# Kernel optimization log

Hardware: AMD Instinct MI355X
Metric: run time of the kernel (lower is better)

Reference implementation:

```python
import jax, jax.numpy as jnp
import numpy as np

B, T, C, H = 64, 512, 384, 64

def setup_inputs() -> dict:
    key = jax.random.key(0)
    ks = jax.random.split(key, 7)
    s = 0.02
    return {
        "x": jax.random.normal(ks[0], (B, T, C), dtype=jnp.float32),
        "Wq": jax.random.normal(ks[1], (C, H), dtype=jnp.float32) * s,
        "bq": jax.random.normal(ks[2], (H,), dtype=jnp.float32) * s,
        "Wk": jax.random.normal(ks[3], (C, H), dtype=jnp.float32) * s,
        "bk": jax.random.normal(ks[4], (H,), dtype=jnp.float32) * s,
        "Wv": jax.random.normal(ks[5], (C, H), dtype=jnp.float32) * s,
        "bv": jax.random.normal(ks[6], (H,), dtype=jnp.float32) * s,
    }

def reference(x, Wq, bq, Wk, bk, Wv, bv):
    # single-head causal self-attention (dropout in eval mode -> identity)
    q = x @ Wq + bq                      # [B,T,H]
    k = x @ Wk + bk                      # [B,T,H]
    v = x @ Wv + bv                      # [B,T,H]
    scale = jnp.asarray(k.shape[-1], x.dtype) ** -0.5
    scores = jnp.einsum('bth,bsh->bts', q, k) * scale   # [B,T,T]
    t = scores.shape[-1]
    causal = jnp.tril(jnp.ones((t, t), dtype=bool))
    scores = jnp.where(causal, scores, jnp.asarray(-jnp.inf, scores.dtype))
    attn = jax.nn.softmax(scores, axis=-1)               # [B,T,T]
    out = jnp.einsum('bts,bsh->bth', attn, v)            # [B,T,H]
    return out
```

## Files before the change

### kernel.cpp

```cpp
#include <hip/hip_runtime.h>
#include <math.h>

#define BB 64
#define TT 512
#define CC 384
#define HH 64
#define MM (BB*TT)

#define QSCALE 0.18033688011112042f

typedef __attribute__((ext_vector_type(8))) short short8;
typedef __attribute__((ext_vector_type(4))) float f32x4;

__device__ __forceinline__ unsigned short f2bf(float f) {
    union { float f; unsigned int u; } x; x.f = f;
    unsigned int r = x.u + 0x7fff + ((x.u >> 16) & 1);
    return (unsigned short)(r >> 16);
}

__global__ __launch_bounds__(256) void prep_w(
    const float* __restrict__ Wq, const float* __restrict__ Wk,
    const float* __restrict__ Wv, unsigned short* __restrict__ Wt)
{
    __shared__ float t[64][65];
    const int which = blockIdx.x / 6;
    const int kt    = blockIdx.x % 6;
    const float* W = (which == 0) ? Wq : (which == 1) ? Wk : Wv;
    const float sc = (which == 0) ? QSCALE : 1.f;
    const int tid = threadIdx.x;
    #pragma unroll
    for (int i = 0; i < 16; i++) {
        int idx = tid + i * 256;
        int kl = idx >> 6, n = idx & 63;
        t[kl][n] = W[(size_t)(kt * 64 + kl) * HH + n];
    }
    __syncthreads();
    #pragma unroll
    for (int i = 0; i < 16; i++) {
        int idx = tid + i * 256;
        int nl = idx >> 6, kl = idx & 63;
        Wt[(size_t)(which * 64 + nl) * CC + kt * 64 + kl] = f2bf(t[kl][nl] * sc);
    }
}

__global__ __launch_bounds__(256) void qkv_proj_mfma(
    const float* __restrict__ x, const unsigned short* __restrict__ Wt,
    const float* __restrict__ bq, const float* __restrict__ bk,
    const float* __restrict__ bv,
    unsigned short* __restrict__ qb, unsigned short* __restrict__ kb,
    unsigned short* __restrict__ vt)
{
    __shared__ unsigned short xs[64][CC + 8];
    const int tid  = threadIdx.x;
    const int w    = tid >> 6;
    const int lane = tid & 63;
    const int l15  = lane & 15;
    const int lg   = lane >> 4;
    const int rows0 = blockIdx.x * 64;

    #pragma unroll
    for (int kc = 0; kc < 6; kc++) {
        #pragma unroll
        for (int i = 0; i < 4; i++) {
            int idx = tid + i * 256;
            int row = idx >> 4, j4 = idx & 15;
            const float4 xv = *reinterpret_cast<const float4*>(
                &x[(size_t)(rows0 + row) * CC + kc * 64 + j4 * 4]);
            ushort4 pk;
            pk.x = f2bf(xv.x); pk.y = f2bf(xv.y);
            pk.z = f2bf(xv.z); pk.w = f2bf(xv.w);
            *reinterpret_cast<ushort4*>(&xs[row][kc * 64 + j4 * 4]) = pk;
        }
    }
    __syncthreads();

    f32x4 acc[4][3];
    #pragma unroll
    for (int mi = 0; mi < 4; mi++)
        #pragma unroll
        for (int f = 0; f < 3; f++) acc[mi][f] = (f32x4){0.f, 0.f, 0.f, 0.f};

    #pragma unroll 4
    for (int ks = 0; ks < 12; ks++) {
        short8 afrag[4];
        #pragma unroll
        for (int mi = 0; mi < 4; mi++)
            afrag[mi] = *reinterpret_cast<const short8*>(
                &xs[mi * 16 + l15][ks * 32 + lg * 8]);
        #pragma unroll
        for (int f = 0; f < 3; f++) {
            const int n = w * 48 + f * 16 + l15;
            const short8 bfrag = *reinterpret_cast<const short8*>(
                &Wt[(size_t)n * CC + ks * 32 + lg * 8]);
            #pragma unroll
            for (int mi = 0; mi < 4; mi++)
                acc[mi][f] = __builtin_amdgcn_mfma_f32_16x16x32_bf16(
                    afrag[mi], bfrag, acc[mi][f], 0, 0, 0);
        }
    }

    const int batch = rows0 >> 9;
    const int t0    = rows0 & 511;

    __syncthreads();
    unsigned short (*L)[72] = reinterpret_cast<unsigned short (*)[72]>(&xs[0][0]);

    #pragma unroll
    for (int f = 0; f < 3; f++) {
        const int c = w * 48 + f * 16 + l15;
        if (c < 64) {
            const float bb = bq[c] * QSCALE;
            #pragma unroll
            for (int mi = 0; mi < 4; mi++)
                #pragma unroll
                for (int rr = 0; rr < 4; rr++)
                    L[mi * 16 + lg * 4 + rr][c] = f2bf(acc[mi][f][rr] + bb);
        } else if (c < 128) {
            const int ci = c - 64;
            const float bb = bk[ci];
            #pragma unroll
            for (int mi = 0; mi < 4; mi++)
                #pragma unroll
                for (int rr = 0; rr < 4; rr++)
                    L[64 + mi * 16 + lg * 4 + rr][ci] = f2bf(acc[mi][f][rr] + bb);
        } else {
            const int ci = c - 128;
            const float bb = bv[ci];
            #pragma unroll
            for (int mi = 0; mi < 4; mi++) {
                ushort4 pk;
                pk.x = f2bf(acc[mi][f][0] + bb);
                pk.y = f2bf(acc[mi][f][1] + bb);
                pk.z = f2bf(acc[mi][f][2] + bb);
                pk.w = f2bf(acc[mi][f][3] + bb);
                *reinterpret_cast<ushort4*>(
                    &vt[((size_t)batch * HH + ci) * TT + t0 + mi * 16 + lg * 4]) = pk;
            }
        }
    }
    __syncthreads();

    #pragma unroll
    for (int i = 0; i < 4; i++) {
        int idx = tid + i * 256;
        int r = idx >> 3, c8 = idx & 7;
        const short8 val = *reinterpret_cast<const short8*>(&L[r][c8 * 8]);
        if (r < 64)
            *reinterpret_cast<short8*>(&qb[(size_t)(rows0 + r) * HH + c8 * 8]) = val;
        else
            *reinterpret_cast<short8*>(&kb[(size_t)(rows0 + r - 64) * HH + c8 * 8]) = val;
    }
}

__global__ __launch_bounds__(256, 3) void attn_mfma(
    const unsigned short* __restrict__ q, const unsigned short* __restrict__ k,
    const unsigned short* __restrict__ vt, float* __restrict__ out)
{
    __shared__ float Cmb[4][16][68];
    __shared__ float Ls[4][16];
    __shared__ unsigned short P[4][16][72];
    const int tid  = threadIdx.x;
    const int w    = tid >> 6;
    const int lane = tid & 63;
    const int l15  = lane & 15;
    const int lg   = lane >> 4;
    const int qs   = blockIdx.x >> 6;
    const int b    = blockIdx.x & 63;
    const int qr0  = b * TT + qs * 16;
    const int n    = (qs >> 2) + 1;

    const unsigned short* __restrict__ kbase = k  + (size_t)b * TT * HH;
    const unsigned short* __restrict__ vbase = vt + (size_t)b * HH * TT;

    short8 aq[2];
    #pragma unroll
    for (int ks = 0; ks < 2; ks++)
        aq[ks] = *reinterpret_cast<const short8*>(
            &q[(size_t)(qr0 + l15) * HH + ks * 32 + lg * 8]);

    f32x4 accO[4];
    #pragma unroll
    for (int nf = 0; nf < 4; nf++) accO[nf] = (f32x4){0.f, 0.f, 0.f, 0.f};
    float lsum[4] = {0.f, 0.f, 0.f, 0.f};

    for (int j = w; j < n; j += 4) {
        short8 kf[2][4];
        #pragma unroll
        for (int ks = 0; ks < 2; ks++)
            #pragma unroll
            for (int nf = 0; nf < 4; nf++)
                kf[ks][nf] = *reinterpret_cast<const short8*>(
                    &kbase[(size_t)(j * 64 + nf * 16 + l15) * HH + ks * 32 + lg * 8]);
        f32x4 s[4];
        #pragma unroll
        for (int nf = 0; nf < 4; nf++) s[nf] = (f32x4){0.f, 0.f, 0.f, 0.f};
        #pragma unroll
        for (int ks = 0; ks < 2; ks++)
            #pragma unroll
            for (int nf = 0; nf < 4; nf++)
                s[nf] = __builtin_amdgcn_mfma_f32_16x16x32_bf16(
                    aq[ks], kf[ks][nf], s[nf], 0, 0, 0);

        short8 vf[2][4];
        #pragma unroll
        for (int ks = 0; ks < 2; ks++)
            #pragma unroll
            for (int nf = 0; nf < 4; nf++)
                vf[ks][nf] = *reinterpret_cast<const short8*>(
                    &vbase[(size_t)(nf * 16 + l15) * TT + j * 64 + ks * 32 + lg * 8]);

        float p[4][4];
        if (j == n - 1) {
            #pragma unroll
            for (int nf = 0; nf < 4; nf++)
                #pragma unroll
                for (int rg = 0; rg < 4; rg++)
                    p[nf][rg] = (j * 64 + nf * 16 + l15 > qs * 16 + lg * 4 + rg)
                                ? 0.f : exp2f(s[nf][rg]);
        } else {
            #pragma unroll
            for (int nf = 0; nf < 4; nf++)
                #pragma unroll
                for (int rg = 0; rg < 4; rg++)
                    p[nf][rg] = exp2f(s[nf][rg]);
        }
        #pragma unroll
        for (int rg = 0; rg < 4; rg++)
            lsum[rg] += (p[0][rg] + p[1][rg]) + (p[2][rg] + p[3][rg]);

        #pragma unroll
        for (int nf = 0; nf < 4; nf++)
            #pragma unroll
            for (int rg = 0; rg < 4; rg++)
                P[w][lg * 4 + rg][nf * 16 + l15] = f2bf(p[nf][rg]);

        #pragma unroll
        for (int ks = 0; ks < 2; ks++) {
            const short8 pa = *reinterpret_cast<const short8*>(
                &P[w][l15][ks * 32 + lg * 8]);
            #pragma unroll
            for (int nf = 0; nf < 4; nf++)
                accO[nf] = __builtin_amdgcn_mfma_f32_16x16x32_bf16(
                    pa, vf[ks][nf], accO[nf], 0, 0, 0);
        }
    }

    #pragma unroll
    for (int rg = 0; rg < 4; rg++) {
        float l = lsum[rg];
        l += __shfl_xor(l, 1);
        l += __shfl_xor(l, 2);
        l += __shfl_xor(l, 4);
        l += __shfl_xor(l, 8);
        if (l15 == 0) Ls[w][lg * 4 + rg] = l;
    }
    #pragma unroll
    for (int nf = 0; nf < 4; nf++)
        #pragma unroll
        for (int rg = 0; rg < 4; rg++)
            Cmb[w][lg * 4 + rg][nf * 16 + l15] = accO[nf][rg];
    __syncthreads();

    #pragma unroll
    for (int rg = 0; rg < 4; rg++) {
        const int row = lg * 4 + rg;
        const float ltot = Ls[0][row] + Ls[1][row] + Ls[2][row] + Ls[3][row];
        const float sum = Cmb[0][row][w * 16 + l15] + Cmb[1][row][w * 16 + l15]
                        + Cmb[2][row][w * 16 + l15] + Cmb[3][row][w * 16 + l15];
        out[(size_t)(qr0 + row) * HH + w * 16 + l15] = sum / ltot;
    }
}

extern "C" void kernel_launch(void* const* d_in, const int* in_sizes, int n_in,
                              void* d_out, int out_size, void* d_ws, size_t ws_size,
                              hipStream_t stream) {
    const float* x  = (const float*)d_in[0];
    const float* Wq = (const float*)d_in[1];
    const float* bq = (const float*)d_in[2];
    const float* Wk = (const float*)d_in[3];
    const float* bk = (const float*)d_in[4];
    const float* Wv = (const float*)d_in[5];
    const float* bv = (const float*)d_in[6];
    float* out = (float*)d_out;

    unsigned short* qb = (unsigned short*)d_ws;
    unsigned short* kb = qb + (size_t)MM * HH;
    unsigned short* vt = kb + (size_t)MM * HH;
    unsigned short* Wt = vt + (size_t)MM * HH;

    prep_w<<<dim3(18), dim3(256), 0, stream>>>(Wq, Wk, Wv, Wt);
    qkv_proj_mfma<<<dim3(MM / 64), dim3(256), 0, stream>>>(
        x, Wt, bq, bk, bv, qb, kb, vt);
    attn_mfma<<<dim3(2048), dim3(256), 0, stream>>>(qb, kb, vt, out);
}
```

Measured before the change: 51.77 us.

## Stage weight tiles in LDS alongside x in two K-halves for QKV projection

The QKV projection kernel now splits the K dimension into two halves of 192. For each half it stages both the bf16-converted x tile and the matching transposed weight slab in shared memory, then runs the MFMA loop reading B fragments from LDS instead of strided global loads. It also switches the float-to-bf16 conversion to the HIP intrinsic. LDS use grows to about 100KB per block, which may reduce occupancy, and an extra barrier is added between the halves.

```diff
diff --git a/kernel.cpp b/kernel.cpp
--- a/kernel.cpp
+++ b/kernel.cpp
@@ -1,4 +1,5 @@
 #include <hip/hip_runtime.h>
+#include <hip/hip_bf16.h>
 #include <math.h>
 
 #define BB 64
@@ -16,6 +17,11 @@
     union { float f; unsigned int u; } x; x.f = f;
     unsigned int r = x.u + 0x7fff + ((x.u >> 16) & 1);
     return (unsigned short)(r >> 16);
+}
+
+__device__ __forceinline__ unsigned short bfc(float f) {
+    __hip_bfloat16 h = __float2bfloat16(f);
+    return *reinterpret_cast<unsigned short*>(&h);
 }
 
 __global__ __launch_bounds__(256) void prep_w(
@@ -50,7 +56,9 @@
     unsigned short* __restrict__ qb, unsigned short* __restrict__ kb,
     unsigned short* __restrict__ vt)
 {
-    __shared__ unsigned short xs[64][CC + 8];
+    __shared__ unsigned short lds[64 * 200 + 192 * 200];
+#define XS(r, c) lds[(r) * 200 + (c)]
+#define WS(r, c) lds[12800 + (r) * 200 + (c)]
     const int tid  = threadIdx.x;
     const int w    = tid >> 6;
     const int lane = tid & 63;
@@ -58,52 +66,62 @@
     const int lg   = lane >> 4;
     const int rows0 = blockIdx.x * 64;
 
-    #pragma unroll
-    for (int kc = 0; kc < 6; kc++) {
-        #pragma unroll
-        for (int i = 0; i < 4; i++) {
-            int idx = tid + i * 256;
-            int row = idx >> 4, j4 = idx & 15;
+    f32x4 acc[4][3];
+    #pragma unroll
+    for (int mi = 0; mi < 4; mi++)
+        #pragma unroll
+        for (int f = 0; f < 3; f++) acc[mi][f] = (f32x4){0.f, 0.f, 0.f, 0.f};
+
+    #pragma unroll 1
+    for (int kh = 0; kh < 2; kh++) {
+        if (kh) __syncthreads();
+
+        #pragma unroll
+        for (int i = 0; i < 12; i++) {
+            int idx = i * 256 + tid;
+            int row = idx / 48, q = idx % 48;
             const float4 xv = *reinterpret_cast<const float4*>(
-                &x[(size_t)(rows0 + row) * CC + kc * 64 + j4 * 4]);
+                &x[(size_t)(rows0 + row) * CC + kh * 192 + q * 4]);
             ushort4 pk;
-            pk.x = f2bf(xv.x); pk.y = f2bf(xv.y);
-            pk.z = f2bf(xv.z); pk.w = f2bf(xv.w);
-            *reinterpret_cast<ushort4*>(&xs[row][kc * 64 + j4 * 4]) = pk;
-        }
-    }
-    __syncthreads();
-
-    f32x4 acc[4][3];
-    #pragma unroll
-    for (int mi = 0; mi < 4; mi++)
-        #pragma unroll
-        for (int f = 0; f < 3; f++) acc[mi][f] = (f32x4){0.f, 0.f, 0.f, 0.f};
-
-    #pragma unroll 4
-    for (int ks = 0; ks < 12; ks++) {
-        short8 afrag[4];
-        #pragma unroll
-        for (int mi = 0; mi < 4; mi++)
-            afrag[mi] = *reinterpret_cast<const short8*>(
-                &xs[mi * 16 + l15][ks * 32 + lg * 8]);
-        #pragma unroll
-        for (int f = 0; f < 3; f++) {
-            const int n = w * 48 + f * 16 + l15;
-            const short8 bfrag = *reinterpret_cast<const short8*>(
-                &Wt[(size_t)n * CC + ks * 32 + lg * 8]);
+            pk.x = bfc(xv.x); pk.y = bfc(xv.y);
+            pk.z = bfc(xv.z); pk.w = bfc(xv.w);
+            *reinterpret_cast<ushort4*>(&XS(row, q * 4)) = pk;
+        }
+        #pragma unroll
+        for (int i = 0; i < 18; i++) {
+            int idx = i * 256 + tid;
+            int row = idx / 24, c8 = idx % 24;
+            *reinterpret_cast<short8*>(&WS(row, c8 * 8)) =
+                *reinterpret_cast<const short8*>(&Wt[(size_t)row * CC + kh * 192 + c8 * 8]);
+        }
+        __syncthreads();
+
+        #pragma unroll
+        for (int ks = 0; ks < 6; ks++) {
+            short8 afrag[4];
             #pragma unroll
             for (int mi = 0; mi < 4; mi++)
-                acc[mi][f] = __builtin_amdgcn_mfma_f32_16x16x32_bf16(
-                    afrag[mi], bfrag, acc[mi][f], 0, 0, 0);
-        }
-    }
+                afrag[mi] = *reinterpret_cast<const short8*>(
+                    &XS(mi * 16 + l15, ks * 32 + lg * 8));
+            #pragma unroll
+            for (int f = 0; f < 3; f++) {
+                const short8 bfrag = *reinterpret_cast<const short8*>(
+                    &WS(w * 48 + f * 16 + l15, ks * 32 + lg * 8));
+                #pragma unroll
+                for (int mi = 0; mi < 4; mi++)
+                    acc[mi][f] = __builtin_amdgcn_mfma_f32_16x16x32_bf16(
+                        afrag[mi], bfrag, acc[mi][f], 0, 0, 0);
+            }
+        }
+    }
+#undef XS
+#undef WS
 
     const int batch = rows0 >> 9;
     const int t0    = rows0 & 511;
 
     __syncthreads();
-    unsigned short (*L)[72] = reinterpret_cast<unsigned short (*)[72]>(&xs[0][0]);
+    unsigned short (*L)[72] = reinterpret_cast<unsigned short (*)[72]>(&lds[0]);
 
     #pragma unroll
     for (int f = 0; f < 3; f++) {
```

Result: slower. 76.11 us (+47.0%).
